# Kernel optimization log

Measured on AMD Instinct MI355X. Metric: run time of the kernel, lower is better.

## Reference

```python
import jax, jax.numpy as jnp
import numpy as np

V, E, H, T = 50000, 128, 256, 9
H2 = H // 2
B, S = 128, 512


def setup_inputs() -> dict:
    key = jax.random.key(0)
    ks = jax.random.split(key, 12)
    sc = 0.05
    return {
        "x": jax.random.randint(ks[0], (B, S), 0, V, dtype=jnp.int64) if False else jax.random.randint(ks[0], (B, S), 0, V).astype(jnp.int64),
        "mask": jnp.ones((B, S), dtype=jnp.int32),
        "embed": jax.random.normal(ks[1], (V, E), jnp.float32) * sc,
        "W_ih_f": jax.random.normal(ks[2], (4 * H2, E), jnp.float32) * sc,
        "W_hh_f": jax.random.normal(ks[3], (4 * H2, H2), jnp.float32) * sc,
        "b_f": jax.random.normal(ks[4], (4 * H2,), jnp.float32) * sc,
        "W_ih_b": jax.random.normal(ks[5], (4 * H2, E), jnp.float32) * sc,
        "W_hh_b": jax.random.normal(ks[6], (4 * H2, H2), jnp.float32) * sc,
        "b_b": jax.random.normal(ks[7], (4 * H2,), jnp.float32) * sc,
        "W_out": jax.random.normal(ks[8], (T, H), jnp.float32) * sc,
        "b_out": jax.random.normal(ks[9], (T,), jnp.float32) * sc,
        "start_trans": jax.random.normal(ks[10], (T,), jnp.float32) * sc,
        "trans": jax.random.normal(ks[11], (T, T), jnp.float32) * sc,
        "end_trans": jax.random.normal(jax.random.fold_in(key, 99), (T,), jnp.float32) * sc,
    }


def _lstm_dir(xg, W_hh, reverse):
    # xg: [B,S,4*H2] precomputed input projections (+bias)
    if reverse:
        xg = xg[:, ::-1]
    b = xg.shape[0]
    h0 = jnp.zeros((b, H2), xg.dtype)

    def step(carry, xt):
        h, c = carry
        g = xt + h @ W_hh.T
        i, f, gg, o = jnp.split(g, 4, axis=-1)
        c = jax.nn.sigmoid(f) * c + jax.nn.sigmoid(i) * jnp.tanh(gg)
        h = jax.nn.sigmoid(o) * jnp.tanh(c)
        return (h, c), h

    _, hs = jax.lax.scan(step, (h0, h0), jnp.swapaxes(xg, 0, 1))
    hs = jnp.swapaxes(hs, 0, 1)  # [B,S,H2]
    if reverse:
        hs = hs[:, ::-1]
    return hs


def _emissions(x, embed, W_ih_f, W_hh_f, b_f, W_ih_b, W_hh_b, b_b, W_out, b_out):
    emb = embed[x]  # [B,S,E]
    xg_f = jnp.einsum('bse,ge->bsg', emb, W_ih_f) + b_f
    xg_b = jnp.einsum('bse,ge->bsg', emb, W_ih_b) + b_b
    h_f = _lstm_dir(xg_f, W_hh_f, False)
    h_b = _lstm_dir(xg_b, W_hh_b, True)
    feats = jnp.concatenate([h_f, h_b], axis=-1)  # [B,S,H]
    return jnp.einsum('bsh,th->bst', feats, W_out) + b_out  # [B,S,T]


def _viterbi(emissions, mask, start_trans, trans, end_trans):
    # emissions [B,S,T], mask [B,S] (1 = valid prefix)
    m = mask.astype(bool)
    score0 = start_trans + emissions[:, 0]  # [B,T]

    def fwd_step(score, inp):
        em_t, m_t = inp  # [B,T], [B]
        nxt = score[:, :, None] + trans[None] + em_t[:, None, :]  # [B,prev,next]
        best = nxt.max(axis=1)
        idx = nxt.argmax(axis=1).astype(jnp.int32)  # [B,T] backpointers
        score = jnp.where(m_t[:, None], best, score)
        return score, idx

    em_rest = jnp.swapaxes(emissions[:, 1:], 0, 1)  # [S-1,B,T]
    m_rest = jnp.swapaxes(m[:, 1:], 0, 1)  # [S-1,B]
    score, history = jax.lax.scan(fwd_step, score0, (em_rest, m_rest))
    final = score + end_trans
    best_scores = final.max(axis=-1)  # [B]
    cur = final.argmax(axis=-1).astype(jnp.int32)  # [B] tag at last valid step

    def back_step(cur, inp):
        hist_t, m_t = inp  # [B,T], [B]
        tag = jnp.where(m_t, cur, -1)  # -1 pads positions beyond seq end
        prev = jnp.take_along_axis(hist_t, cur[:, None], axis=1)[:, 0]
        cur = jnp.where(m_t, prev, cur)
        return cur, tag

    cur0, tags_rev = jax.lax.scan(back_step, cur, (history[::-1], m_rest[::-1]))
    paths = jnp.concatenate(
        [cur0[:, None], jnp.swapaxes(tags_rev, 0, 1)[:, ::-1]], axis=1)  # [B,S]
    return paths, best_scores


def reference(x, mask, embed, W_ih_f, W_hh_f, b_f, W_ih_b, W_hh_b, b_b,
              W_out, b_out, start_trans, trans, end_trans):
    emissions = _emissions(x, embed, W_ih_f, W_hh_f, b_f,
                           W_ih_b, W_hh_b, b_b, W_out, b_out)
    paths, best_scores = _viterbi(emissions, mask, start_trans, trans, end_trans)
    return paths, best_scores
```

## Files before the change

### kernel.cpp

```cpp
#include <hip/hip_runtime.h>
#include <stdint.h>

#define S_LEN 512
#define NT 9

typedef __attribute__((ext_vector_type(8)))  short          bf16x8;
typedef __attribute__((ext_vector_type(4)))  float          f32x4;
typedef __attribute__((ext_vector_type(4)))  unsigned short u16x4;
typedef __attribute__((ext_vector_type(4)))  unsigned int   u32x4;

static __device__ __forceinline__ unsigned short f2bf(float f) {
    union { float f; unsigned u; } c; c.f = f;
    return (unsigned short)((c.u + 0x7fffu + ((c.u >> 16) & 1u)) >> 16);
}
static __device__ __forceinline__ float bf2f(unsigned short h) {
    union { unsigned u; float f; } c; c.u = ((unsigned)h) << 16;
    return c.f;
}
static __device__ __forceinline__ bf16x8 cvt8(const float* p) {
    f32x4 a = *(const f32x4*)p, b = *(const f32x4*)(p + 4);
    bf16x8 fr;
    fr[0]=(short)f2bf(a[0]); fr[1]=(short)f2bf(a[1]); fr[2]=(short)f2bf(a[2]); fr[3]=(short)f2bf(a[3]);
    fr[4]=(short)f2bf(b[0]); fr[5]=(short)f2bf(b[1]); fr[6]=(short)f2bf(b[2]); fr[7]=(short)f2bf(b[3]);
    return fr;
}
static __device__ __forceinline__ float sigf(float x) {
    return __builtin_amdgcn_rcpf(1.0f + __expf(-x));
}
static __device__ __forceinline__ float tanhf_(float x) {
    return 1.0f - 2.0f * __builtin_amdgcn_rcpf(1.0f + __expf(2.0f * x));
}

static __device__ __forceinline__ void wg_barrier_lds() {
    asm volatile("s_waitcnt lgkmcnt(0)" ::: "memory");
    __builtin_amdgcn_s_barrier();
    asm volatile("" ::: "memory");
}

__global__ __launch_bounds__(512) void k_xg(
    const int* __restrict__ x, const float* __restrict__ embed,
    const float* __restrict__ Wf, const float* __restrict__ bF,
    const float* __restrict__ Wb, const float* __restrict__ bB,
    unsigned short* __restrict__ xg)
{
    const int dir = blockIdx.y, s = blockIdx.x;
    const float* __restrict__ W    = dir ? Wb : Wf;
    const float* __restrict__ bias = dir ? bB : bF;
    const int tid = threadIdx.x;
    const int wv = tid >> 6, L = tid & 63, l15 = L & 15, l4 = L >> 4;

    bf16x8 Bf[4][4];
    float  bq[4];
#pragma unroll
    for (int q = 0; q < 4; ++q) {
        const int gate = q * 128 + wv * 16 + l15;
        bq[q] = bias[gate];
#pragma unroll
        for (int kt = 0; kt < 4; ++kt)
            Bf[q][kt] = cvt8(W + gate * 128 + kt * 32 + l4 * 8);
    }

    __shared__ int tokL[128];
    __shared__ unsigned short stage[16384];

    if (tid < 128) tokL[tid] = x[tid * S_LEN + s];
    const int srow0 = tid >> 5, scol = tid & 31;
    __syncthreads();

#pragma unroll
    for (int ch = 0; ch < 2; ++ch) {
        f32x4 vv[4];
#pragma unroll
        for (int i = 0; i < 4; ++i)
            vv[i] = *(const f32x4*)(embed + (size_t)tokL[(ch*4+i)*16 + srow0] * 128 + scol * 4);
#pragma unroll
        for (int i = 0; i < 4; ++i) {
            const int row = (ch*4+i)*16 + srow0;
            unsigned short b4[4];
            b4[0]=f2bf(vv[i][0]); b4[1]=f2bf(vv[i][1]); b4[2]=f2bf(vv[i][2]); b4[3]=f2bf(vv[i][3]);
            int byte = row * 256 + ((scol * 8) ^ ((row & 7) << 4));
            *(uint2*)((char*)stage + byte) = *(const uint2*)b4;
        }
    }
    __syncthreads();

    const int hc = wv * 16 + l15;

    for (int bt16 = 0; bt16 < 8; ++bt16) {
        bf16x8 A[4];
#pragma unroll
        for (int kt = 0; kt < 4; ++kt) {
            int byte = (bt16 * 16 + l15) * 256 + ((kt * 64 + l4 * 16) ^ ((l15 & 7) << 4));
            A[kt] = *(const bf16x8*)((const char*)stage + byte);
        }
        f32x4 acc[4];
#pragma unroll
        for (int q = 0; q < 4; ++q) {
            f32x4 a0 = { bq[q], bq[q], bq[q], bq[q] };
#pragma unroll
            for (int kt = 0; kt < 4; ++kt)
                a0 = __builtin_amdgcn_mfma_f32_16x16x32_bf16(A[kt], Bf[q][kt], a0, 0, 0, 0);
            acc[q] = a0;
        }
#pragma unroll
        for (int j = 0; j < 4; ++j) {
            u16x4 sv;
#pragma unroll
            for (int q = 0; q < 4; ++q) sv[q] = f2bf(acc[q][j]);
            unsigned short* dst = xg +
                (((size_t)s * 2 + dir) * 128 + bt16 * 16 + l4 * 4 + j) * 512 + hc * 4;
            *(u16x4*)dst = sv;
        }
    }
}

__global__ __launch_bounds__(512) void k_lstm(
    const unsigned short* __restrict__ xg,
    const float* __restrict__ Whf, const float* __restrict__ Whb,
    unsigned short* __restrict__ feats)
{
    const int dir = blockIdx.y, bt = blockIdx.x;
    const float* __restrict__ Wh = dir ? Whb : Whf;
    const int tid = threadIdx.x, w = tid >> 6, L = tid & 63, l15 = L & 15, l4 = L >> 4;

    bf16x8 Bf[4][4];
#pragma unroll
    for (int q = 0; q < 4; ++q)
#pragma unroll
        for (int kt = 0; kt < 4; ++kt)
            Bf[q][kt] = cvt8(Wh + (q * 128 + w * 16 + l15) * 128 + kt * 32 + l4 * 8);

    __shared__ unsigned short hl[2048];
    for (int i = tid; i < 1024; i += 512) ((unsigned*)hl)[i] = 0;

    const int ar = l15 >> 2;
    int rdoff[4];
#pragma unroll
    for (int kt = 0; kt < 4; ++kt) {
        int p = (kt * 4 + l4 + 2 * ar) & 15;
        rdoff[kt] = ar * 256 + p * 16;
    }
    const int hc = w * 16 + l15;
    const int wroff = l4 * 256 + (((hc >> 3) + 2 * l4) & 15) * 16 + (hc & 7) * 2;

    float c = 0.f;
    const size_t xoff = ((size_t)(bt * 4 + l4)) * 512 + hc * 4;
    const unsigned short* xp = xg + xoff + (size_t)dir * 65536;
    unsigned short* fcur = feats + ((size_t)(bt * 4 + l4) * 512 + (dir ? 511 : 0)) * 256
                                 + dir * 128 + hc;
    const ptrdiff_t fstep = dir ? -256 : 256;

    u16x4 xvA = *(const u16x4*)(xp + (size_t)(dir ? 511 : 0) * 131072);
    u16x4 xvB = *(const u16x4*)(xp + (size_t)(dir ? 510 : 1) * 131072);

    f32x4 acc[4];
#pragma unroll
    for (int q = 0; q < 4; ++q) acc[q] = f32x4{0.f, 0.f, 0.f, 0.f};

    __syncthreads();

#define LSTM_STEP(T, XV)                                                        \
    {                                                                           \
        const int t_ = (T);                                                     \
        const char* bufR = (const char*)hl + (t_ & 1) * 1024;                   \
        char*       bufW = (char*)hl + ((t_ & 1) ^ 1) * 1024;                   \
        const int tc_ = (t_ + 2 < 511) ? (t_ + 2) : 511;       \
        const int s2_ = dir ? (511 - tc_) : tc_;             \
        u16x4 xnew = *(const u16x4*)(xp + (size_t)s2_ * 131072);                \
        bf16x8 A_[4];                                                           \
        _Pragma("unroll")                                                       \
        for (int kt = 0; kt < 4; ++kt)                                          \
            A_[kt] = *(const bf16x8*)(bufR + rdoff[kt]);                        \
        __builtin_amdgcn_s_setprio(1);                                          \
        _Pragma("unroll")                                                       \
        for (int q = 0; q < 4; ++q) {                                           \
            acc[q][0] = bf2f(XV[q]);                                            \
            _Pragma("unroll")                                                   \
            for (int kt = 0; kt < 4; ++kt)                                      \
                acc[q] = __builtin_amdgcn_mfma_f32_16x16x32_bf16(               \
                             A_[kt], Bf[q][kt], acc[q], 0, 0, 0);               \
        }                                                                       \
        __builtin_amdgcn_s_setprio(0);                                          \
        float ig = sigf(acc[0][0]);                                             \
        float fg = sigf(acc[1][0]);                                             \
        float gg = tanhf_(acc[2][0]);                                           \
        float og = sigf(acc[3][0]);                                             \
        c = fg * c + ig * gg;                                                   \
        float h_ = og * tanhf_(c);                                              \
        unsigned short hb = f2bf(h_);                                           \
        *(unsigned short*)(bufW + wroff) = hb;                                  \
        *fcur = hb; fcur += fstep;                                              \
        wg_barrier_lds();                                                       \
        XV = xnew;                                                              \
    }

    for (int it = 0; it < 256; ++it) {
        LSTM_STEP(2 * it,     xvA)
        LSTM_STEP(2 * it + 1, xvB)
    }
#undef LSTM_STEP
}

__global__ __launch_bounds__(256) void k_emis(
    const unsigned short* __restrict__ feats,
    const float* __restrict__ Wout, float* __restrict__ emp)
{
    const int tid = threadIdx.x;
    const int wid = blockIdx.x * 4 + (tid >> 6);
    const int L = tid & 63, l15 = L & 15, l4 = L >> 4;
    const int b = wid >> 5, sg = wid & 31;

    bf16x8 Of[2][4];
#pragma unroll
    for (int d = 0; d < 2; ++d)
#pragma unroll
        for (int kt = 0; kt < 4; ++kt) { bf16x8 z;
#pragma unroll
            for (int i = 0; i < 8; ++i) z[i] = 0; Of[d][kt] = z; }
    if (l15 < NT) {
#pragma unroll
        for (int d = 0; d < 2; ++d)
#pragma unroll
            for (int kt = 0; kt < 4; ++kt)
                Of[d][kt] = cvt8(Wout + l15 * 256 + d * 128 + kt * 32 + l4 * 8);
    }

    const unsigned short* frow = feats + ((size_t)b * 512 + sg * 16 + l15) * 256;
#pragma unroll
    for (int d = 0; d < 2; ++d) {
        bf16x8 A[4];
#pragma unroll
        for (int kt = 0; kt < 4; ++kt)
            A[kt] = *(const bf16x8*)(frow + d * 128 + kt * 32 + l4 * 8);
        f32x4 em0 = {0, 0, 0, 0};
#pragma unroll
        for (int kt = 0; kt < 4; ++kt)
            em0 = __builtin_amdgcn_mfma_f32_16x16x32_bf16(A[kt], Of[d][kt], em0, 0, 0, 0);
        if (l15 < NT) {
#pragma unroll
            for (int j = 0; j < 4; ++j)
                emp[((size_t)(d * 128 + b) * 512 + sg * 16 + l4 * 4 + j) * 9 + l15] = em0[j];
        }
    }
}

__global__ __launch_bounds__(256) void k_viterbi(
    const float* __restrict__ emp, const int* __restrict__ mask,
    const float* __restrict__ bout, const float* __restrict__ startt,
    const float* __restrict__ trans, const float* __restrict__ endt,
    float* __restrict__ out)
{
    const int b = blockIdx.x, tid = threadIdx.x;
    __shared__ float em[512 * 9];
    __shared__ int   msk[512];
    __shared__ unsigned char hist[512 * 9];
    __shared__ unsigned char Gl[32 * 12];
    __shared__ unsigned char bound[32];
    __shared__ int curS;

    const float* pf = emp + (size_t)b * 4608;
    const float* pb = emp + (size_t)(128 + b) * 4608;
    for (int i = tid; i < 4608; i += 256) {
        unsigned q = ((unsigned)i * 7282u) >> 16;
        em[i] = pf[i] + pb[i] + bout[i - 9 * q];
    }
    for (int i = tid; i < 512; i += 256) msk[i] = mask[b * 512 + i];
    __syncthreads();

    if (tid < 64) {
        const int k = (tid < NT) ? tid : 0;
        float trk[9];
#pragma unroll
        for (int j = 0; j < NT; ++j) trk[j] = trans[j * 9 + k];
        float score = startt[k] + em[k];
        for (int t = 1; t < 512; ++t) {
            float v[9];
#pragma unroll
            for (int j = 0; j < NT; ++j) v[j] = __shfl(score, j, 64) + trk[j];
            float m01 = fmaxf(v[0], v[1]), m23 = fmaxf(v[2], v[3]);
            float m45 = fmaxf(v[4], v[5]), m67 = fmaxf(v[6], v[7]);
            float m = fmaxf(fmaxf(fmaxf(m01, m23), fmaxf(m45, m67)), v[8]);
            int bi = 0;
#pragma unroll
            for (int j = 8; j >= 0; --j) if (v[j] == m) bi = j;
            if (msk[t]) score = m + em[t * 9 + k];
            if (tid < NT) hist[t * 9 + tid] = (unsigned char)bi;
        }
        float fin = score + endt[k];
        float bs = -3e38f; int cur = 0;
#pragma unroll
        for (int j = 0; j < NT; ++j) {
            float vv = __shfl(fin, j, 64);
            if (vv > bs) { bs = vv; cur = j; }
        }
        if (tid == 0) { curS = cur; out[65536 + b] = bs; }
    }
    __syncthreads();

    if (tid < 32) {
        const int m = tid;
        int G[9];
#pragma unroll
        for (int k = 0; k < NT; ++k) G[k] = k;
        const int hi = (m == 31) ? 511 : (16 * m + 16);
        for (int t = hi; t >= 16 * m + 1; --t) {
            if (msk[t]) {
#pragma unroll
                for (int k = 0; k < NT; ++k) G[k] = hist[t * 9 + G[k]];
            }
        }
#pragma unroll
        for (int k = 0; k < NT; ++k) Gl[m * 12 + k] = (unsigned char)G[k];
    }
    __syncthreads();

    if (tid == 0) {
        int e = curS;
        bound[31] = (unsigned char)e;
        for (int m = 31; m >= 1; --m) { e = Gl[m * 12 + e]; bound[m - 1] = (unsigned char)e; }
        out[(size_t)b * 512] = (float)Gl[0 * 12 + e];
    }
    __syncthreads();

    if (tid < 32) {
        const int m = tid;
        int ccur = bound[m];
        const int hi = (m == 31) ? 511 : (16 * m + 16);
        for (int t = hi; t >= 16 * m + 1; --t) {
            const int mt = msk[t];
            out[(size_t)b * 512 + t] = (float)(mt ? ccur : -1);
            if (mt) ccur = hist[t * 9 + ccur];
        }
    }
}

extern "C" void kernel_launch(void* const* d_in, const int* in_sizes, int n_in,
                              void* d_out, int out_size, void* d_ws, size_t ws_size,
                              hipStream_t stream) {
    const int*   x      = (const int*)d_in[0];
    const int*   mask   = (const int*)d_in[1];
    const float* embed  = (const float*)d_in[2];
    const float* Wihf   = (const float*)d_in[3];
    const float* Whhf   = (const float*)d_in[4];
    const float* bf_    = (const float*)d_in[5];
    const float* Wihb   = (const float*)d_in[6];
    const float* Whhb   = (const float*)d_in[7];
    const float* bb_    = (const float*)d_in[8];
    const float* Wout   = (const float*)d_in[9];
    const float* bout   = (const float*)d_in[10];
    const float* startt = (const float*)d_in[11];
    const float* trans  = (const float*)d_in[12];
    const float* endt   = (const float*)d_in[13];

    unsigned short* xg    = (unsigned short*)d_ws;
    float*          emp   = (float*)((char*)d_ws + (size_t)134217728);
    unsigned short* feats = (unsigned short*)((char*)d_ws + (size_t)138936320);
    float*          out   = (float*)d_out;

    k_xg     <<<dim3(512, 2), 512, 0, stream>>>(x, embed, Wihf, bf_, Wihb, bb_, xg);
    k_lstm   <<<dim3(32, 2),  512, 0, stream>>>(xg, Whhf, Whhb, feats);
    k_emis   <<<1024,         256, 0, stream>>>(feats, Wout, emp);
    k_viterbi<<<128,          256, 0, stream>>>(emp, mask, bout, startt, trans, endt, out);
}
```

Before: 416.6 us.

## Fuse emission projection into Viterbi and merge both directions in xg kernel

The emissions matmul kernel is removed and its MFMA projection moves into the Viterbi kernel, which writes emissions straight to LDS. This drops one launch and the global round trip of the emission partials. The xg kernel now processes both LSTM directions in one 1024-thread block, so the embedding gather and bf16 staging happen once per timestep instead of twice. The LSTM step also drops its s_setprio calls. The Viterbi prologue grows, and the larger xg block needs more registers per block.

After: 561.5 us. 34.8% more time.

```diff
diff --git a/kernel.cpp b/kernel.cpp
--- a/kernel.cpp
+++ b/kernel.cpp
@@ -7,7 +7,6 @@
 typedef __attribute__((ext_vector_type(8)))  short          bf16x8;
 typedef __attribute__((ext_vector_type(4)))  float          f32x4;
 typedef __attribute__((ext_vector_type(4)))  unsigned short u16x4;
-typedef __attribute__((ext_vector_type(4)))  unsigned int   u32x4;
 
 static __device__ __forceinline__ unsigned short f2bf(float f) {
     union { float f; unsigned u; } c; c.f = f;
@@ -37,17 +36,30 @@
     asm volatile("" ::: "memory");
 }
 
-__global__ __launch_bounds__(512) void k_xg(
+__global__ __launch_bounds__(1024) void k_xg(
     const int* __restrict__ x, const float* __restrict__ embed,
     const float* __restrict__ Wf, const float* __restrict__ bF,
     const float* __restrict__ Wb, const float* __restrict__ bB,
     unsigned short* __restrict__ xg)
 {
-    const int dir = blockIdx.y, s = blockIdx.x;
+    const int s = blockIdx.x;
+    const int tid = threadIdx.x;
+    const int w16 = tid >> 6, L = tid & 63, l15 = L & 15, l4 = L >> 4;
+    const int dir = w16 >> 3, wv = w16 & 7;
     const float* __restrict__ W    = dir ? Wb : Wf;
     const float* __restrict__ bias = dir ? bB : bF;
-    const int tid = threadIdx.x;
-    const int wv = tid >> 6, L = tid & 63, l15 = L & 15, l4 = L >> 4;
+
+    __shared__ int tokL[128];
+    __shared__ unsigned short stage[16384];
+
+    if (tid < 128) tokL[tid] = x[tid * S_LEN + s];
+    const int srow = tid >> 5, scol = tid & 31;
+    __syncthreads();
+
+    f32x4 vv[4];
+#pragma unroll
+    for (int p = 0; p < 4; ++p)
+        vv[p] = *(const f32x4*)(embed + (size_t)tokL[p * 32 + srow] * 128 + scol * 4);
 
     bf16x8 Bf[4][4];
     float  bq[4];
@@ -60,27 +72,13 @@
             Bf[q][kt] = cvt8(W + gate * 128 + kt * 32 + l4 * 8);
     }
 
-    __shared__ int tokL[128];
-    __shared__ unsigned short stage[16384];
-
-    if (tid < 128) tokL[tid] = x[tid * S_LEN + s];
-    const int srow0 = tid >> 5, scol = tid & 31;
-    __syncthreads();
-
-#pragma unroll
-    for (int ch = 0; ch < 2; ++ch) {
-        f32x4 vv[4];
-#pragma unroll
-        for (int i = 0; i < 4; ++i)
-            vv[i] = *(const f32x4*)(embed + (size_t)tokL[(ch*4+i)*16 + srow0] * 128 + scol * 4);
-#pragma unroll
-        for (int i = 0; i < 4; ++i) {
-            const int row = (ch*4+i)*16 + srow0;
-            unsigned short b4[4];
-            b4[0]=f2bf(vv[i][0]); b4[1]=f2bf(vv[i][1]); b4[2]=f2bf(vv[i][2]); b4[3]=f2bf(vv[i][3]);
-            int byte = row * 256 + ((scol * 8) ^ ((row & 7) << 4));
-            *(uint2*)((char*)stage + byte) = *(const uint2*)b4;
-        }
+#pragma unroll
+    for (int p = 0; p < 4; ++p) {
+        const int row = p * 32 + srow;
+        unsigned short b4[4];
+        b4[0]=f2bf(vv[p][0]); b4[1]=f2bf(vv[p][1]); b4[2]=f2bf(vv[p][2]); b4[3]=f2bf(vv[p][3]);
+        int byte = row * 256 + ((scol * 8) ^ ((row & 7) << 4));
+        *(uint2*)((char*)stage + byte) = *(const uint2*)b4;
     }
     __syncthreads();
 
@@ -164,14 +162,13 @@
         const int t_ = (T);                                                     \
         const char* bufR = (const char*)hl + (t_ & 1) * 1024;                   \
         char*       bufW = (char*)hl + ((t_ & 1) ^ 1) * 1024;                   \
-        const int tc_ = (t_ + 2 < 511) ? (t_ + 2) : 511;       \
-        const int s2_ = dir ? (511 - tc_) : tc_;             \
+        const int tc_ = (t_ < 510) ? (t_ + 2) : t_;                             \
+        const int s2_ = dir ? (511 - tc_) : tc_;                                \
         u16x4 xnew = *(const u16x4*)(xp + (size_t)s2_ * 131072);                \
         bf16x8 A_[4];                                                           \
         _Pragma("unroll")                                                       \
         for (int kt = 0; kt < 4; ++kt)                                          \
             A_[kt] = *(const bf16x8*)(bufR + rdoff[kt]);                        \
-        __builtin_amdgcn_s_setprio(1);                                          \
         _Pragma("unroll")                                                       \
         for (int q = 0; q < 4; ++q) {                                           \
             acc[q][0] = bf2f(XV[q]);                                            \
@@ -180,7 +177,6 @@
                 acc[q] = __builtin_amdgcn_mfma_f32_16x16x32_bf16(               \
                              A_[kt], Bf[q][kt], acc[q], 0, 0, 0);               \
         }                                                                       \
-        __builtin_amdgcn_s_setprio(0);                                          \
         float ig = sigf(acc[0][0]);                                             \
         float fg = sigf(acc[1][0]);                                             \
         float gg = tanhf_(acc[2][0]);                                           \
@@ -201,56 +197,14 @@
 #undef LSTM_STEP
 }
 
-__global__ __launch_bounds__(256) void k_emis(
-    const unsigned short* __restrict__ feats,
-    const float* __restrict__ Wout, float* __restrict__ emp)
-{
-    const int tid = threadIdx.x;
-    const int wid = blockIdx.x * 4 + (tid >> 6);
-    const int L = tid & 63, l15 = L & 15, l4 = L >> 4;
-    const int b = wid >> 5, sg = wid & 31;
-
-    bf16x8 Of[2][4];
-#pragma unroll
-    for (int d = 0; d < 2; ++d)
-#pragma unroll
-        for (int kt = 0; kt < 4; ++kt) { bf16x8 z;
-#pragma unroll
-            for (int i = 0; i < 8; ++i) z[i] = 0; Of[d][kt] = z; }
-    if (l15 < NT) {
-#pragma unroll
-        for (int d = 0; d < 2; ++d)
-#pragma unroll
-            for (int kt = 0; kt < 4; ++kt)
-                Of[d][kt] = cvt8(Wout + l15 * 256 + d * 128 + kt * 32 + l4 * 8);
-    }
-
-    const unsigned short* frow = feats + ((size_t)b * 512 + sg * 16 + l15) * 256;
-#pragma unroll
-    for (int d = 0; d < 2; ++d) {
-        bf16x8 A[4];
-#pragma unroll
-        for (int kt = 0; kt < 4; ++kt)
-            A[kt] = *(const bf16x8*)(frow + d * 128 + kt * 32 + l4 * 8);
-        f32x4 em0 = {0, 0, 0, 0};
-#pragma unroll
-        for (int kt = 0; kt < 4; ++kt)
-            em0 = __builtin_amdgcn_mfma_f32_16x16x32_bf16(A[kt], Of[d][kt], em0, 0, 0, 0);
-        if (l15 < NT) {
-#pragma unroll
-            for (int j = 0; j < 4; ++j)
-                emp[((size_t)(d * 128 + b) * 512 + sg * 16 + l4 * 4 + j) * 9 + l15] = em0[j];
-        }
-    }
-}
-
 __global__ __launch_bounds__(256) void k_viterbi(
-    const float* __restrict__ emp, const int* __restrict__ mask,
-    const float* __restrict__ bout, const float* __restrict__ startt,
-    const float* __restrict__ trans, const float* __restrict__ endt,
-    float* __restrict__ out)
+    const unsigned short* __restrict__ feats, const float* __restrict__ Wout,
+    const int* __restrict__ mask, const float* __restrict__ bout,
+    const float* __restrict__ startt, const float* __restrict__ trans,
+    const float* __restrict__ endt, float* __restrict__ out)
 {
     const int b = blockIdx.x, tid = threadIdx.x;
+    const int w = tid >> 6, L = tid & 63, l15 = L & 15, l4 = L >> 4;
     __shared__ float em[512 * 9];
     __shared__ int   msk[512];
     __shared__ unsigned char hist[512 * 9];
@@ -258,13 +212,46 @@
     __shared__ unsigned char bound[32];
     __shared__ int curS;
 
-    const float* pf = emp + (size_t)b * 4608;
-    const float* pb = emp + (size_t)(128 + b) * 4608;
-    for (int i = tid; i < 4608; i += 256) {
-        unsigned q = ((unsigned)i * 7282u) >> 16;
-        em[i] = pf[i] + pb[i] + bout[i - 9 * q];
-    }
+    bf16x8 Of[2][4];
+#pragma unroll
+    for (int d = 0; d < 2; ++d)
+#pragma unroll
+        for (int kt = 0; kt < 4; ++kt) { bf16x8 z;
+#pragma unroll
+            for (int i = 0; i < 8; ++i) z[i] = 0; Of[d][kt] = z; }
+    float bv = 0.f;
+    if (l15 < NT) {
+        bv = bout[l15];
+#pragma unroll
+        for (int d = 0; d < 2; ++d)
+#pragma unroll
+            for (int kt = 0; kt < 4; ++kt)
+                Of[d][kt] = cvt8(Wout + l15 * 256 + d * 128 + kt * 32 + l4 * 8);
+    }
+
     for (int i = tid; i < 512; i += 256) msk[i] = mask[b * 512 + i];
+
+#pragma unroll
+    for (int i = 0; i < 8; ++i) {
+        const int sg = w * 8 + i;
+        const unsigned short* frow = feats + ((size_t)b * 512 + sg * 16 + l15) * 256;
+        f32x4 e0 = {0, 0, 0, 0}, e1 = {0, 0, 0, 0};
+#pragma unroll
+        for (int kt = 0; kt < 4; ++kt) {
+            bf16x8 A = *(const bf16x8*)(frow + kt * 32 + l4 * 8);
+            e0 = __builtin_amdgcn_mfma_f32_16x16x32_bf16(A, Of[0][kt], e0, 0, 0, 0);
+        }
+#pragma unroll
+        for (int kt = 0; kt < 4; ++kt) {
+            bf16x8 A = *(const bf16x8*)(frow + 128 + kt * 32 + l4 * 8);
+            e1 = __builtin_amdgcn_mfma_f32_16x16x32_bf16(A, Of[1][kt], e1, 0, 0, 0);
+        }
+        if (l15 < NT) {
+#pragma unroll
+            for (int j = 0; j < 4; ++j)
+                em[(sg * 16 + l4 * 4 + j) * 9 + l15] = (e0[j] + e1[j]) + bv;
+        }
+    }
     __syncthreads();
 
     if (tid < 64) {
@@ -353,12 +340,10 @@
     const float* endt   = (const float*)d_in[13];
 
     unsigned short* xg    = (unsigned short*)d_ws;
-    float*          emp   = (float*)((char*)d_ws + (size_t)134217728);
-    unsigned short* feats = (unsigned short*)((char*)d_ws + (size_t)138936320);
+    unsigned short* feats = (unsigned short*)((char*)d_ws + (size_t)134217728);
     float*          out   = (float*)d_out;
 
-    k_xg     <<<dim3(512, 2), 512, 0, stream>>>(x, embed, Wihf, bf_, Wihb, bb_, xg);
-    k_lstm   <<<dim3(32, 2),  512, 0, stream>>>(xg, Whhf, Whhb, feats);
-    k_emis   <<<1024,         256, 0, stream>>>(feats, Wout, emp);
-    k_viterbi<<<128,          256, 0, stream>>>(emp, mask, bout, startt, trans, endt, out);
-}
+    k_xg     <<<512,          1024, 0, stream>>>(x, embed, Wihf, bf_, Wihb, bb_, xg);
+    k_lstm   <<<dim3(32, 2),  512,  0, stream>>>(xg, Whhf, Whhb, feats);
+    k_viterbi<<<128,          256,  0, stream>>>(feats, Wout, mask, bout, startt, trans, endt, out);
+}
```
